# Kernel tuning notes

Measured on AMD Instinct MI355X. Metric: run time of the kernel, lower is better.

Reference implementation:

```python
import jax, jax.numpy as jnp
import numpy as np

B, T, C = 8, 4096, 768


def wkv(w, u, k, v):
    """RWKV WKV linear recurrence with running max/exp state.
    w, u: (C,) ; k, v: (B, T, C) -> y: (B, T, C), all float32.
    Faithful to wkv_pytorch: note w is ADDED to pp (no negation/exp).
    """
    kt = jnp.swapaxes(k, 0, 1)  # (T, B, C)
    vt = jnp.swapaxes(v, 0, 1)

    def step(carry, inp):
        aa, bb, pp = carry            # each (B, C)
        k_t, v_t = inp                # each (B, C)
        ww = u[None, :] + k_t
        p = jnp.maximum(pp, ww)
        e1 = jnp.exp(pp - p)
        e2 = jnp.exp(ww - p)
        y_t = (e1 * aa + e2 * v_t) / (e1 * bb + e2)
        ww2 = w[None, :] + pp
        p2 = jnp.maximum(ww2, k_t)
        e1b = jnp.exp(ww2 - p2)
        e2b = jnp.exp(k_t - p2)
        aa = e1b * aa + e2b * v_t
        bb = e1b * bb + e2b
        return (aa, bb, p2), y_t

    init = (jnp.zeros((B, C), jnp.float32),
            jnp.zeros((B, C), jnp.float32),
            jnp.full((B, C), -1e38, jnp.float32))
    _, y = jax.lax.scan(step, init, (kt, vt))
    return jnp.swapaxes(y, 0, 1)  # (B, T, C)


def setup_inputs() -> dict:
    key = jax.random.key(0)
    ks = jax.random.split(key, 7)
    scale = 1.0 / np.sqrt(C)
    x = jax.random.normal(ks[0], (B, T, C), jnp.float32)
    w_key = jax.random.normal(ks[1], (C, C), jnp.float32) * scale
    w_value = jax.random.normal(ks[2], (C, C), jnp.float32) * scale
    w_receptance = jax.random.normal(ks[3], (C, C), jnp.float32) * scale
    w_output = jax.random.normal(ks[4], (C, C), jnp.float32) * scale
    # 'fancy' init, layer_id=5, n_layer=12
    layer_id, n_layer = 5, 12
    ratio_0_to_1 = layer_id / (n_layer - 1)
    h = np.arange(C, dtype=np.float64)
    spatial_decay = (-5.0 + 8.0 * (h / (C - 1)) ** (0.7 + 1.3 * ratio_0_to_1)).astype(np.float32)
    zigzag = (np.array([(i + 1) % 3 - 1 for i in range(C)], dtype=np.float64) * 0.5)
    spatial_first = (np.ones(C) * np.log(0.3) + zigzag).astype(np.float32)
    return {
        "x": x,
        "w_key": w_key,
        "w_value": w_value,
        "w_receptance": w_receptance,
        "w_output": w_output,
        "spatial_decay": jnp.asarray(spatial_decay),
        "spatial_first": jnp.asarray(spatial_first),
    }


def reference(x, w_key, w_value, w_receptance, w_output, spatial_decay, spatial_first):
    # shift_pixel=0, empty spatial_shift_list -> xk = xv = xr = x
    k = jnp.einsum('btc,oc->bto', x, w_key)
    v = jnp.einsum('btc,oc->bto', x, w_value)
    sr = jax.nn.sigmoid(jnp.einsum('btc,oc->bto', x, w_receptance))
    y = wkv(spatial_decay / T, spatial_first / T, k, v)
    out = jnp.einsum('btc,oc->bto', sr * y, w_output)
    return out
```

## Files before the change

kernel.cpp:

```cpp
#include <hip/hip_runtime.h>
#include <hip/hip_bf16.h>

using bf16 = __hip_bfloat16;
typedef short bf16x8v  __attribute__((ext_vector_type(8)));
typedef float f32x16v  __attribute__((ext_vector_type(16)));

#define GLD_LDS16(g, l) __builtin_amdgcn_global_load_lds(                      \
    (const __attribute__((address_space(1))) void*)(g),                        \
    (__attribute__((address_space(3))) void*)(l), 16, 0, 0)

__device__ __forceinline__ float bflo(unsigned int u) {
  union { unsigned int i; float f; } c; c.i = u << 16; return c.f;
}
__device__ __forceinline__ float bfhi(unsigned int u) {
  union { unsigned int i; float f; } c; c.i = u & 0xffff0000u; return c.f;
}
__device__ __forceinline__ unsigned int packbf(float a, float b) {
  return (unsigned int)(__hip_bfloat16_raw(__float2bfloat16(a)).x) |
         ((unsigned int)(__hip_bfloat16_raw(__float2bfloat16(b)).x) << 16);
}
__device__ __forceinline__ unsigned short bfraw(float a) {
  return __hip_bfloat16_raw(__float2bfloat16(a)).x;
}

__global__ void f2b4_all(const float* __restrict__ x,  const float* __restrict__ wk,
                         const float* __restrict__ wv, const float* __restrict__ wr,
                         const float* __restrict__ wo,
                         bf16* __restrict__ x_bf, bf16* __restrict__ wcat,
                         bf16* __restrict__ wo_bf) {
  int i = blockIdx.x * blockDim.x + threadIdx.x;
  const float* s; bf16* d; int idx;
  if (i < 6291456) { s = x; d = x_bf; idx = i; }
  else {
    int j = i - 6291456;
    int seg = j / 147456;
    idx = j - seg * 147456;
    if (seg == 0)      { s = wk; d = wcat; }
    else if (seg == 1) { s = wv; d = wcat + 589824; }
    else if (seg == 2) { s = wr; d = wcat + 1179648; }
    else               { s = wo; d = wo_bf; }
  }
  const float4 f = reinterpret_cast<const float4*>(s)[idx];
  struct B4 { bf16 a, b, c, d; };
  B4 o = { __float2bfloat16(f.x), __float2bfloat16(f.y),
           __float2bfloat16(f.z), __float2bfloat16(f.w) };
  reinterpret_cast<B4*>(d)[idx] = o;
}

__device__ __forceinline__ void gemm_tile_acc(
    const bf16* __restrict__ A, const bf16* __restrict__ W,
    bf16* lds_a, bf16* lds_b, int tid, size_t m0, int n0, f32x16v acc[2][2])
{
  const int lane = tid & 63;
  const int wave = tid >> 6;
  const int l31  = lane & 31;
  const int hi   = lane >> 5;
  const int wr   = (wave >> 1) * 64;
  const int wc   = (wave & 1) * 64;

  int srow[4], scol[4];
#pragma unroll
  for (int q = 0; q < 4; ++q) {
    const int s = tid + q * 256;
    srow[q] = s >> 3;
    scol[q] = (((s & 7) ^ (srow[q] & 7)) * 8);
  }

#pragma unroll
  for (int i = 0; i < 2; ++i)
#pragma unroll
    for (int j = 0; j < 2; ++j)
#pragma unroll
      for (int r = 0; r < 16; ++r) acc[i][j][r] = 0.0f;

  for (int k0 = 0; k0 < 768; k0 += 64) {
    __syncthreads();
#pragma unroll
    for (int q = 0; q < 4; ++q)
      GLD_LDS16(A + (m0 + srow[q]) * 768 + k0 + scol[q], &lds_a[(size_t)(tid + q * 256) * 8]);
#pragma unroll
    for (int q = 0; q < 4; ++q)
      GLD_LDS16(W + (size_t)(n0 + srow[q]) * 768 + k0 + scol[q], &lds_b[(size_t)(tid + q * 256) * 8]);
    __syncthreads();

#pragma unroll
    for (int ks = 0; ks < 4; ++ks) {
      const int gl = ks * 2 + hi;
      bf16x8v av[2], bv[2];
#pragma unroll
      for (int i = 0; i < 2; ++i) {
        const int ra = wr + 32 * i + l31;
        av[i] = *(const bf16x8v*)&lds_a[ra * 64 + ((gl ^ (ra & 7)) * 8)];
      }
#pragma unroll
      for (int j = 0; j < 2; ++j) {
        const int rb = wc + 32 * j + l31;
        bv[j] = *(const bf16x8v*)&lds_b[rb * 64 + ((gl ^ (rb & 7)) * 8)];
      }
#pragma unroll
      for (int i = 0; i < 2; ++i)
#pragma unroll
        for (int j = 0; j < 2; ++j)
          acc[i][j] = __builtin_amdgcn_mfma_f32_32x32x16_bf16(bv[j], av[i], acc[i][j], 0, 0, 0);
    }
  }
}


__global__ __launch_bounds__(256) void gemm_kvr(
    const bf16* __restrict__ A, const bf16* __restrict__ Wcat,
    bf16* __restrict__ Kb, bf16* __restrict__ Vb, bf16* __restrict__ SRb)
{
  __shared__ __align__(16) bf16 lds_a[128 * 64];
  __shared__ __align__(16) bf16 lds_b[128 * 64];
  const int tid = threadIdx.x;
  const int bx = blockIdx.x;
  const int chunk = bx / 1152;
  const int rem   = bx % 1152;
  const int mm    = rem & 63;
  const int nt    = rem >> 6;
  const size_t m0 = (size_t)(chunk * 64 + mm) * 128;
  const int n0 = nt * 128;

  f32x16v acc[2][2];
  gemm_tile_acc(A, Wcat, lds_a, lds_b, tid, m0, n0, acc);

  const int seg   = n0 / 768;
  const int ncol0 = n0 - seg * 768;
  bf16* __restrict__ dst = (seg == 0) ? Kb : (seg == 1) ? Vb : SRb;
  const int lane = tid & 63, wave = tid >> 6;
  const int l31 = lane & 31, hi = lane >> 5;
  const int wr = (wave >> 1) * 64, wc = (wave & 1) * 64;
#pragma unroll
  for (int i = 0; i < 2; ++i) {
    const size_t mrow = m0 + wr + 32 * i + l31;
#pragma unroll
    for (int j = 0; j < 2; ++j) {
      const int nb = ncol0 + wc + 32 * j + 4 * hi;
#pragma unroll
      for (int rr = 0; rr < 4; ++rr) {
        float v0 = acc[i][j][4 * rr + 0], v1 = acc[i][j][4 * rr + 1];
        float v2 = acc[i][j][4 * rr + 2], v3 = acc[i][j][4 * rr + 3];
        if (seg == 2) {
          v0 = 1.0f / (1.0f + __expf(-v0)); v1 = 1.0f / (1.0f + __expf(-v1));
          v2 = 1.0f / (1.0f + __expf(-v2)); v3 = 1.0f / (1.0f + __expf(-v3));
        }
        ushort4 pk = { bfraw(v0), bfraw(v1), bfraw(v2), bfraw(v3) };
        *(ushort4*)&dst[mrow * 768 + nb + 8 * rr] = pk;
      }
    }
  }
}

__global__ __launch_bounds__(256) void gemm_out(
    const bf16* __restrict__ A, const bf16* __restrict__ W,
    float* __restrict__ out)
{
  __shared__ __align__(16) bf16 lds_a[128 * 64];
  __shared__ __align__(16) bf16 lds_b[128 * 64];
  const int tid = threadIdx.x;
  const int bx = blockIdx.x;
  const int chunk = bx / 384;
  const int rem   = bx % 384;
  const int mm    = rem & 63;
  const int nt    = rem >> 6;
  const size_t m0 = (size_t)(chunk * 64 + mm) * 128;
  const int n0 = nt * 128;

  f32x16v acc[2][2];
  gemm_tile_acc(A, W, lds_a, lds_b, tid, m0, n0, acc);

  const int lane = tid & 63, wave = tid >> 6;
  const int l31 = lane & 31, hi = lane >> 5;
  const int wr = (wave >> 1) * 64, wc = (wave & 1) * 64;
#pragma unroll
  for (int i = 0; i < 2; ++i) {
    const size_t mrow = m0 + wr + 32 * i + l31;
#pragma unroll
    for (int j = 0; j < 2; ++j) {
      const int nb = n0 + wc + 32 * j + 4 * hi;
#pragma unroll
      for (int rr = 0; rr < 4; ++rr) {
        float4 pk = { acc[i][j][4 * rr + 0], acc[i][j][4 * rr + 1],
                      acc[i][j][4 * rr + 2], acc[i][j][4 * rr + 3] };
        *(float4*)&out[mrow * 768 + nb + 8 * rr] = pk;
      }
    }
  }
}

__global__ void wkv_phaseA(const bf16* __restrict__ K, const bf16* __restrict__ V,
                           const float* __restrict__ sd,
                           float* __restrict__ sA, float* __restrict__ sB, float* __restrict__ sP)
{
  const int idx = blockIdx.x * 256 + threadIdx.x;
  const int c4 = idx % 192;
  const int bg = idx / 192;
  const int g  = bg & 127;
  const int b  = bg >> 7;
  const int c0 = c4 * 4;
  float w[4], aa[4], bb[4], pp[4];
#pragma unroll
  for (int e = 0; e < 4; ++e) {
    w[e] = sd[c0 + e] * (1.0f / 4096.0f);
    aa[e] = 0.f; bb[e] = 0.f; pp[e] = -1e38f;
  }
  const size_t base = ((size_t)b * 4096 + (size_t)g * 32) * 768 + c0;
  const uint2* Kp = (const uint2*)(K + base);
  const uint2* Vp = (const uint2*)(V + base);
#pragma unroll 4
  for (int t = 0; t < 32; ++t) {
    const uint2 ku = Kp[(size_t)t * 192];
    const uint2 vu = Vp[(size_t)t * 192];
    const float kc[4] = { bflo(ku.x), bfhi(ku.x), bflo(ku.y), bfhi(ku.y) };
    const float vc[4] = { bflo(vu.x), bfhi(vu.x), bflo(vu.y), bfhi(vu.y) };
#pragma unroll
    for (int e = 0; e < 4; ++e) {
      const float ww2 = w[e] + pp[e];
      const float p2  = fmaxf(ww2, kc[e]);
      const float e1b = __expf(ww2 - p2);
      const float e2b = __expf(kc[e] - p2);
      aa[e] = e1b * aa[e] + e2b * vc[e];
      bb[e] = e1b * bb[e] + e2b;
      pp[e] = p2;
    }
  }
  const int o = g * 6144 + b * 768 + c0;
#pragma unroll
  for (int e = 0; e < 4; ++e) { sA[o + e] = aa[e]; sB[o + e] = bb[e]; sP[o + e] = pp[e]; }
}

__global__ void wkv_phaseB(const float* __restrict__ sA, const float* __restrict__ sB,
                           const float* __restrict__ sP,
                           float* __restrict__ iA, float* __restrict__ iB, float* __restrict__ iP,
                           const float* __restrict__ sd)
{
  const int bc = blockIdx.x * 256 + threadIdx.x;
  const int c  = bc % 768;
  const float Lw = 32.0f * (sd[c] * (1.0f / 4096.0f));
  float aa = 0.f, bb = 0.f, pp = -1e38f;
  for (int g = 0; g < 128; ++g) {
    const int o = g * 6144 + bc;
    iA[o] = aa; iB[o] = bb; iP[o] = pp;
    const float la = sA[o], lb = sB[o], lp = sP[o];
    const float pd = pp + Lw;
    const float pn = fmaxf(pd, lp);
    const float e0 = __expf(pd - pn);
    const float e1 = __expf(lp - pn);
    aa = e0 * aa + e1 * la;
    bb = e0 * bb + e1 * lb;
    pp = pn;
  }
}

__global__ void wkv_phaseC(const bf16* __restrict__ K, const bf16* __restrict__ V,
                           const bf16* __restrict__ SR,
                           const float* __restrict__ iA, const float* __restrict__ iB,
                           const float* __restrict__ iP,
                           const float* __restrict__ sd, const float* __restrict__ sf,
                           bf16* __restrict__ RY)
{
  const int idx = blockIdx.x * 256 + threadIdx.x;
  const int c4 = idx % 192;
  const int bg = idx / 192;
  const int g  = bg & 127;
  const int b  = bg >> 7;
  const int c0 = c4 * 4;
  const int o = g * 6144 + b * 768 + c0;
  float w[4], u[4], aa[4], bb[4], pp[4];
#pragma unroll
  for (int e = 0; e < 4; ++e) {
    w[e] = sd[c0 + e] * (1.0f / 4096.0f);
    u[e] = sf[c0 + e] * (1.0f / 4096.0f);
    aa[e] = iA[o + e]; bb[e] = iB[o + e]; pp[e] = iP[o + e];
  }
  const size_t base = ((size_t)b * 4096 + (size_t)g * 32) * 768 + c0;
  const uint2* Kp = (const uint2*)(K + base);
  const uint2* Vp = (const uint2*)(V + base);
  const uint2* Sp = (const uint2*)(SR + base);
  uint2* Rp = (uint2*)(RY + base);
#pragma unroll 4
  for (int t = 0; t < 32; ++t) {
    const uint2 ku = Kp[(size_t)t * 192];
    const uint2 vu = Vp[(size_t)t * 192];
    const uint2 su = Sp[(size_t)t * 192];
    const float kc[4] = { bflo(ku.x), bfhi(ku.x), bflo(ku.y), bfhi(ku.y) };
    const float vc[4] = { bflo(vu.x), bfhi(vu.x), bflo(vu.y), bfhi(vu.y) };
    const float sc[4] = { bflo(su.x), bfhi(su.x), bflo(su.y), bfhi(su.y) };
    float y[4];
#pragma unroll
    for (int e = 0; e < 4; ++e) {
      const float ww = u[e] + kc[e];
      const float p  = fmaxf(pp[e], ww);
      const float e1 = __expf(pp[e] - p);
      const float e2 = __expf(ww - p);
      y[e] = (e1 * aa[e] + e2 * vc[e]) / (e1 * bb[e] + e2) * sc[e];
      const float ww2 = w[e] + pp[e];
      const float p2  = fmaxf(ww2, kc[e]);
      const float e1b = __expf(ww2 - p2);
      const float e2b = __expf(kc[e] - p2);
      aa[e] = e1b * aa[e] + e2b * vc[e];
      bb[e] = e1b * bb[e] + e2b;
      pp[e] = p2;
    }
    uint2 r; r.x = packbf(y[0], y[1]); r.y = packbf(y[2], y[3]);
    Rp[(size_t)t * 192] = r;
  }
}

extern "C" void kernel_launch(void* const* d_in, const int* in_sizes, int n_in,
                              void* d_out, int out_size, void* d_ws, size_t ws_size,
                              hipStream_t stream)
{
  const float* x  = (const float*)d_in[0];
  const float* wk = (const float*)d_in[1];
  const float* wv = (const float*)d_in[2];
  const float* wr = (const float*)d_in[3];
  const float* wo = (const float*)d_in[4];
  const float* sd = (const float*)d_in[5];
  const float* sf = (const float*)d_in[6];
  float* out = (float*)d_out;

  char* ws = (char*)d_ws;
  bf16*  x_bf  = (bf16*) (ws + 0);
  bf16*  wcat  = (bf16*) (ws + 50331648);
  bf16*  wo_bf = (bf16*) (ws + 53870592);
  bf16*  Kb    = (bf16*) (ws + 55050240);
  bf16*  Vb    = (bf16*) (ws + 105381888);
  bf16*  SRb   = (bf16*) (ws + 155713536);
  float* sumA  = (float*)(ws + 206045184);
  float* sumB  = (float*)(ws + 209190912);
  float* sumP  = (float*)(ws + 212336640);
  float* iniA  = (float*)(ws + 215482368);
  float* iniB  = (float*)(ws + 218628096);
  float* iniP  = (float*)(ws + 221773824);
  bf16*  ry_bf = x_bf;

  f2b4_all<<<26880, 256, 0, stream>>>(x, wk, wv, wr, wo, x_bf, wcat, wo_bf);

  gemm_kvr<<<4608, 256, 0, stream>>>(x_bf, wcat, Kb, Vb, SRb);

  wkv_phaseA<<<768, 256, 0, stream>>>(Kb, Vb, sd, sumA, sumB, sumP);
  wkv_phaseB<<<24,  256, 0, stream>>>(sumA, sumB, sumP, iniA, iniB, iniP, sd);
  wkv_phaseC<<<768, 256, 0, stream>>>(Kb, Vb, SRb, iniA, iniB, iniP, sd, sf, ry_bf);

  gemm_out<<<1536, 256, 0, stream>>>(ry_bf, wo_bf, out);
}
```

Baseline: 475.4 us.

## Use 8-wave GEMM tiles and parallel-scan the WKV chunk-state combine

The two GEMM kernels now launch 512 threads per block. The 128x128 tile is split across 8 waves, each computing 64x32 with two MFMA accumulators instead of four, and each thread issues half as many LDS-staging loads. Phase B of the WKV recurrence, which was a 128-step sequential loop per channel over only 24 blocks, becomes a Hillis-Steele log-step scan in shared memory with one block per (batch, channel) and one thread per chunk. This is meant to add parallelism to the sequential phase and occupancy to the GEMMs, at the cost of less register-level reuse per wave and extra syncthreads in the scan.

```diff
diff --git a/kernel.cpp b/kernel.cpp
--- a/kernel.cpp
+++ b/kernel.cpp
@@ -49,19 +49,19 @@
 
 __device__ __forceinline__ void gemm_tile_acc(
     const bf16* __restrict__ A, const bf16* __restrict__ W,
-    bf16* lds_a, bf16* lds_b, int tid, size_t m0, int n0, f32x16v acc[2][2])
+    bf16* lds_a, bf16* lds_b, int tid, size_t m0, int n0, f32x16v acc[2])
 {
   const int lane = tid & 63;
   const int wave = tid >> 6;
   const int l31  = lane & 31;
   const int hi   = lane >> 5;
-  const int wr   = (wave >> 1) * 64;
-  const int wc   = (wave & 1) * 64;
-
-  int srow[4], scol[4];
-#pragma unroll
-  for (int q = 0; q < 4; ++q) {
-    const int s = tid + q * 256;
+  const int wr   = (wave >> 2) * 64;
+  const int wc   = (wave & 3) * 32;
+
+  int srow[2], scol[2];
+#pragma unroll
+  for (int q = 0; q < 2; ++q) {
+    const int s = tid + q * 512;
     srow[q] = s >> 3;
     scol[q] = (((s & 7) ^ (srow[q] & 7)) * 8);
   }
@@ -69,45 +69,40 @@
 #pragma unroll
   for (int i = 0; i < 2; ++i)
 #pragma unroll
-    for (int j = 0; j < 2; ++j)
-#pragma unroll
-      for (int r = 0; r < 16; ++r) acc[i][j][r] = 0.0f;
+    for (int r = 0; r < 16; ++r) acc[i][r] = 0.0f;
 
   for (int k0 = 0; k0 < 768; k0 += 64) {
     __syncthreads();
 #pragma unroll
-    for (int q = 0; q < 4; ++q)
-      GLD_LDS16(A + (m0 + srow[q]) * 768 + k0 + scol[q], &lds_a[(size_t)(tid + q * 256) * 8]);
-#pragma unroll
-    for (int q = 0; q < 4; ++q)
-      GLD_LDS16(W + (size_t)(n0 + srow[q]) * 768 + k0 + scol[q], &lds_b[(size_t)(tid + q * 256) * 8]);
+    for (int q = 0; q < 2; ++q)
+      GLD_LDS16(A + (m0 + srow[q]) * 768 + k0 + scol[q], &lds_a[(size_t)(tid + q * 512) * 8]);
+#pragma unroll
+    for (int q = 0; q < 2; ++q)
+      GLD_LDS16(W + (size_t)(n0 + srow[q]) * 768 + k0 + scol[q], &lds_b[(size_t)(tid + q * 512) * 8]);
     __syncthreads();
 
 #pragma unroll
     for (int ks = 0; ks < 4; ++ks) {
       const int gl = ks * 2 + hi;
-      bf16x8v av[2], bv[2];
+      bf16x8v av[2], bv;
 #pragma unroll
       for (int i = 0; i < 2; ++i) {
         const int ra = wr + 32 * i + l31;
         av[i] = *(const bf16x8v*)&lds_a[ra * 64 + ((gl ^ (ra & 7)) * 8)];
       }
-#pragma unroll
-      for (int j = 0; j < 2; ++j) {
-        const int rb = wc + 32 * j + l31;
-        bv[j] = *(const bf16x8v*)&lds_b[rb * 64 + ((gl ^ (rb & 7)) * 8)];
+      {
+        const int rb = wc + l31;
+        bv = *(const bf16x8v*)&lds_b[rb * 64 + ((gl ^ (rb & 7)) * 8)];
       }
 #pragma unroll
       for (int i = 0; i < 2; ++i)
-#pragma unroll
-        for (int j = 0; j < 2; ++j)
-          acc[i][j] = __builtin_amdgcn_mfma_f32_32x32x16_bf16(bv[j], av[i], acc[i][j], 0, 0, 0);
-    }
-  }
-}
-
-
-__global__ __launch_bounds__(256) void gemm_kvr(
+        acc[i] = __builtin_amdgcn_mfma_f32_32x32x16_bf16(bv, av[i], acc[i], 0, 0, 0);
+    }
+  }
+}
+
+
+__global__ __launch_bounds__(512) void gemm_kvr(
     const bf16* __restrict__ A, const bf16* __restrict__ Wcat,
     bf16* __restrict__ Kb, bf16* __restrict__ Vb, bf16* __restrict__ SRb)
 {
@@ -122,7 +117,7 @@
   const size_t m0 = (size_t)(chunk * 64 + mm) * 128;
   const int n0 = nt * 128;
 
-  f32x16v acc[2][2];
+  f32x16v acc[2];
   gemm_tile_acc(A, Wcat, lds_a, lds_b, tid, m0, n0, acc);
 
   const int seg   = n0 / 768;
@@ -130,29 +125,26 @@
   bf16* __restrict__ dst = (seg == 0) ? Kb : (seg == 1) ? Vb : SRb;
   const int lane = tid & 63, wave = tid >> 6;
   const int l31 = lane & 31, hi = lane >> 5;
-  const int wr = (wave >> 1) * 64, wc = (wave & 1) * 64;
+  const int wr = (wave >> 2) * 64, wc = (wave & 3) * 32;
 #pragma unroll
   for (int i = 0; i < 2; ++i) {
     const size_t mrow = m0 + wr + 32 * i + l31;
-#pragma unroll
-    for (int j = 0; j < 2; ++j) {
-      const int nb = ncol0 + wc + 32 * j + 4 * hi;
-#pragma unroll
-      for (int rr = 0; rr < 4; ++rr) {
-        float v0 = acc[i][j][4 * rr + 0], v1 = acc[i][j][4 * rr + 1];
-        float v2 = acc[i][j][4 * rr + 2], v3 = acc[i][j][4 * rr + 3];
-        if (seg == 2) {
-          v0 = 1.0f / (1.0f + __expf(-v0)); v1 = 1.0f / (1.0f + __expf(-v1));
-          v2 = 1.0f / (1.0f + __expf(-v2)); v3 = 1.0f / (1.0f + __expf(-v3));
-        }
-        ushort4 pk = { bfraw(v0), bfraw(v1), bfraw(v2), bfraw(v3) };
-        *(ushort4*)&dst[mrow * 768 + nb + 8 * rr] = pk;
+    const int nb = ncol0 + wc + 4 * hi;
+#pragma unroll
+    for (int rr = 0; rr < 4; ++rr) {
+      float v0 = acc[i][4 * rr + 0], v1 = acc[i][4 * rr + 1];
+      float v2 = acc[i][4 * rr + 2], v3 = acc[i][4 * rr + 3];
+      if (seg == 2) {
+        v0 = 1.0f / (1.0f + __expf(-v0)); v1 = 1.0f / (1.0f + __expf(-v1));
+        v2 = 1.0f / (1.0f + __expf(-v2)); v3 = 1.0f / (1.0f + __expf(-v3));
       }
-    }
-  }
-}
-
-__global__ __launch_bounds__(256) void gemm_out(
+      ushort4 pk = { bfraw(v0), bfraw(v1), bfraw(v2), bfraw(v3) };
+      *(ushort4*)&dst[mrow * 768 + nb + 8 * rr] = pk;
+    }
+  }
+}
+
+__global__ __launch_bounds__(512) void gemm_out(
     const bf16* __restrict__ A, const bf16* __restrict__ W,
     float* __restrict__ out)
 {
@@ -167,24 +159,21 @@
   const size_t m0 = (size_t)(chunk * 64 + mm) * 128;
   const int n0 = nt * 128;
 
-  f32x16v acc[2][2];
+  f32x16v acc[2];
   gemm_tile_acc(A, W, lds_a, lds_b, tid, m0, n0, acc);
 
   const int lane = tid & 63, wave = tid >> 6;
   const int l31 = lane & 31, hi = lane >> 5;
-  const int wr = (wave >> 1) * 64, wc = (wave & 1) * 64;
+  const int wr = (wave >> 2) * 64, wc = (wave & 3) * 32;
 #pragma unroll
   for (int i = 0; i < 2; ++i) {
     const size_t mrow = m0 + wr + 32 * i + l31;
-#pragma unroll
-    for (int j = 0; j < 2; ++j) {
-      const int nb = n0 + wc + 32 * j + 4 * hi;
-#pragma unroll
-      for (int rr = 0; rr < 4; ++rr) {
-        float4 pk = { acc[i][j][4 * rr + 0], acc[i][j][4 * rr + 1],
-                      acc[i][j][4 * rr + 2], acc[i][j][4 * rr + 3] };
-        *(float4*)&out[mrow * 768 + nb + 8 * rr] = pk;
-      }
+    const int nb = n0 + wc + 4 * hi;
+#pragma unroll
+    for (int rr = 0; rr < 4; ++rr) {
+      float4 pk = { acc[i][4 * rr + 0], acc[i][4 * rr + 1],
+                    acc[i][4 * rr + 2], acc[i][4 * rr + 3] };
+      *(float4*)&out[mrow * 768 + nb + 8 * rr] = pk;
     }
   }
 }
@@ -235,22 +224,36 @@
                            float* __restrict__ iA, float* __restrict__ iB, float* __restrict__ iP,
                            const float* __restrict__ sd)
 {
-  const int bc = blockIdx.x * 256 + threadIdx.x;
+  const int bc = blockIdx.x;
+  const int g  = threadIdx.x;
   const int c  = bc % 768;
   const float Lw = 32.0f * (sd[c] * (1.0f / 4096.0f));
-  float aa = 0.f, bb = 0.f, pp = -1e38f;
-  for (int g = 0; g < 128; ++g) {
-    const int o = g * 6144 + bc;
-    iA[o] = aa; iB[o] = bb; iP[o] = pp;
-    const float la = sA[o], lb = sB[o], lp = sP[o];
-    const float pd = pp + Lw;
-    const float pn = fmaxf(pd, lp);
-    const float e0 = __expf(pd - pn);
-    const float e1 = __expf(lp - pn);
-    aa = e0 * aa + e1 * la;
-    bb = e0 * bb + e1 * lb;
-    pp = pn;
-  }
+  __shared__ float sa[128], sb[128], sp[128], sl[128];
+  const int o = g * 6144 + bc;
+  float a = sA[o], b = sB[o], p = sP[o], L = Lw;
+  sa[g] = a; sb[g] = b; sp[g] = p; sl[g] = L;
+  __syncthreads();
+#pragma unroll
+  for (int d = 1; d < 128; d <<= 1) {
+    float a2 = a, b2 = b, p2 = p, L2 = L;
+    if (g >= d) {
+      const float al = sa[g - d], bl = sb[g - d], pl = sp[g - d], Ll = sl[g - d];
+      const float pn = fmaxf(pl + L, p);
+      const float e0 = __expf(pl + L - pn);
+      const float e1 = __expf(p - pn);
+      a2 = e0 * al + e1 * a;
+      b2 = e0 * bl + e1 * b;
+      p2 = pn;
+      L2 = Ll + L;
+    }
+    __syncthreads();
+    sa[g] = a2; sb[g] = b2; sp[g] = p2; sl[g] = L2;
+    a = a2; b = b2; p = p2; L = L2;
+    __syncthreads();
+  }
+  float oa = 0.f, ob = 0.f, op = -1e38f;
+  if (g > 0) { oa = sa[g - 1]; ob = sb[g - 1]; op = sp[g - 1]; }
+  iA[o] = oa; iB[o] = ob; iP[o] = op;
 }
 
 __global__ void wkv_phaseC(const bf16* __restrict__ K, const bf16* __restrict__ V,
@@ -338,11 +341,11 @@
 
   f2b4_all<<<26880, 256, 0, stream>>>(x, wk, wv, wr, wo, x_bf, wcat, wo_bf);
 
-  gemm_kvr<<<4608, 256, 0, stream>>>(x_bf, wcat, Kb, Vb, SRb);
+  gemm_kvr<<<4608, 512, 0, stream>>>(x_bf, wcat, Kb, Vb, SRb);
 
   wkv_phaseA<<<768, 256, 0, stream>>>(Kb, Vb, sd, sumA, sumB, sumP);
-  wkv_phaseB<<<24,  256, 0, stream>>>(sumA, sumB, sumP, iniA, iniB, iniP, sd);
+  wkv_phaseB<<<6144, 128, 0, stream>>>(sumA, sumB, sumP, iniA, iniB, iniP, sd);
   wkv_phaseC<<<768, 256, 0, stream>>>(Kb, Vb, SRb, iniA, iniB, iniP, sd, sf, ry_bf);
 
-  gemm_out<<<1536, 256, 0, stream>>>(ry_bf, wo_bf, out);
-}
+  gemm_out<<<1536, 512, 0, stream>>>(ry_bf, wo_bf, out);
+}
```

Result: slower. 498.2 us (+4.8%).
